# Kernel tuning notes

Hardware: AMD Instinct MI355X
Metric: run time of the kernel (lower is better)

## Reference

```python
import jax, jax.numpy as jnp
import numpy as np

K_MASK = -2.3819763e+38
B, T, D, N, K, H = 2, 4096, 2048, 8, 1, 256


def apply_rope(inputs, positions, head_dim):
    # inputs: [B, T, n, H], positions: [B, T]
    fraction = 2.0 * jnp.arange(0, head_dim // 2, dtype=jnp.float32) / head_dim
    timescale = 10000.0 ** fraction  # [H/2]
    sinusoid_inp = positions[..., None].astype(jnp.float32) / timescale  # [B,T,H/2]
    sinusoid_inp = sinusoid_inp[..., None, :]  # [B,T,1,H/2]
    sin, cos = jnp.sin(sinusoid_inp), jnp.cos(sinusoid_inp)
    first_half, second_half = jnp.split(inputs, 2, axis=-1)
    first_part = first_half * cos - second_half * sin
    second_part = second_half * cos + first_half * sin
    return jnp.concatenate([first_part, second_part], axis=-1).astype(inputs.dtype)


def setup_inputs() -> dict:
    key = jax.random.key(0)
    kx, kq, kkv, ko = jax.random.split(key, 4)
    x = jax.random.normal(kx, (B, T, D), dtype=jnp.float32)
    segment_pos = jnp.broadcast_to(jnp.arange(T, dtype=jnp.int32), (B, T))
    attn_mask = jnp.broadcast_to(
        jnp.tril(jnp.ones((T, T), dtype=bool)), (B, T, T))  # causal
    q_w = jax.random.normal(kq, (N, D, H), dtype=jnp.float32) * 0.02
    kv_w = jax.random.normal(kkv, (2, K, D, H), dtype=jnp.float32) * 0.02
    out_w = jax.random.normal(ko, (N, H, D), dtype=jnp.float32) * 0.02
    return {"x": x, "segment_pos": segment_pos, "attn_mask": attn_mask,
            "q_w": q_w, "kv_w": kv_w, "out_w": out_w}


def reference(x, segment_pos, attn_mask, q_w, kv_w, out_w):
    # Projections (GQA branch: num_kv_heads != num_heads)
    query_proj = jnp.einsum('btd,ndh->btnh', x, q_w)          # [B,T,N,H]
    kv_proj = jnp.einsum('bsd,ckdh->cbskh', x, kv_w)          # [2,B,T,K,H]
    key_proj, value_proj = kv_proj[0], kv_proj[1]

    query_proj = apply_rope(query_proj, segment_pos, head_dim=H)
    query_scaled = query_proj * H ** (-0.5)
    key_proj = apply_rope(key_proj, segment_pos, head_dim=H)

    # Repeat KV heads for GQA (num_kv_heads == 1 -> N heads)
    value_proj = jnp.repeat(value_proj, N, axis=-2)           # [B,S,N,H]
    key_proj = jnp.repeat(key_proj, N, axis=-2)               # [B,S,N,H]

    logits = jnp.einsum('btnh,bsnh->btns', query_scaled, key_proj)
    padded_logits = jnp.where(attn_mask[:, :, None, :], logits, K_MASK)
    probs = jax.nn.softmax(padded_logits, axis=-1).astype(key_proj.dtype)
    encoded = jnp.einsum('btns,bsnh->btnh', probs, value_proj)
    attn_output = jnp.einsum('btnh,nhd->btd', encoded, out_w)
    return attn_output
```

## Files before the change

### kernel.cpp

```cpp
#include <hip/hip_runtime.h>

#define T_SEQ 4096
#define D_MODEL 2048
#define N_HEADS 8
#define HDIM 256

typedef unsigned int uint32;
typedef unsigned short u16;
typedef __attribute__((ext_vector_type(8))) short short8;
typedef __attribute__((ext_vector_type(4))) float f32x4;
typedef __attribute__((ext_vector_type(4))) uint32 u32x4;

__device__ __forceinline__ float bf2f(u16 v) {
  return __uint_as_float(((uint32)v) << 16);
}
__device__ __forceinline__ u16 f2bf(float f) {
  uint32 u = __float_as_uint(f);
  u += 0x7fffu + ((u >> 16) & 1u);
  return (u16)(u >> 16);
}
__device__ __forceinline__ uint32 pkbf(float x, float y) {
  return (uint32)f2bf(x) | ((uint32)f2bf(y) << 16);
}
__device__ __forceinline__ uint2 pack4(const f32x4 v) {
  uint2 r;
  r.x = (uint32)f2bf(v[0]) | ((uint32)f2bf(v[1]) << 16);
  r.y = (uint32)f2bf(v[2]) | ((uint32)f2bf(v[3]) << 16);
  return r;
}
__device__ __forceinline__ void gload16(const u16* g, u16* l) {
  __builtin_amdgcn_global_load_lds(
      (const __attribute__((address_space(1))) unsigned int*)g,
      (__attribute__((address_space(3))) unsigned int*)l, 16, 0, 0);
}

__global__ __launch_bounds__(256) void convert_x(const float* __restrict__ x,
                                                 u16* __restrict__ xb) {
  const int idx = blockIdx.x * 256 + threadIdx.x;
  float4 v = *(const float4*)(x + (size_t)idx * 4);
  uint2 pk;
  pk.x = (uint32)f2bf(v.x) | ((uint32)f2bf(v.y) << 16);
  pk.y = (uint32)f2bf(v.z) | ((uint32)f2bf(v.w) << 16);
  *(uint2*)(xb + (size_t)idx * 4) = pk;
}

__global__ __launch_bounds__(256) void prep_weights(
    const float* __restrict__ qw, const float* __restrict__ kvw,
    const float* __restrict__ ow, u16* __restrict__ Wt, u16* __restrict__ Owt) {
  __shared__ float Ts[64][65];
  const int t = threadIdx.x;
  const int tx = blockIdx.x, ty = blockIdx.y, z = blockIdx.z;
  const float* src;
  int srcStride;
  u16* dst;
  if (z == 0) {
    const int c0 = tx * 64;
    const float* base = (c0 < 2048)
                            ? qw + (size_t)(c0 >> 8) * D_MODEL * HDIM
                            : kvw + (size_t)((c0 - 2048) >> 8) * D_MODEL * HDIM;
    src = base + (c0 & 255);
    srcStride = HDIM;
    dst = Wt + (size_t)c0 * D_MODEL;
  } else {
    if (tx >= 32) return;
    src = ow + tx * 64;
    srcStride = D_MODEL;
    dst = Owt + (size_t)tx * 64 * D_MODEL;
  }
  const int d0 = ty * 64;
  const int r = t >> 4, c4 = (t & 15) * 4;
#pragma unroll
  for (int i = 0; i < 4; ++i) {
    float4 v = *(const float4*)(src + (size_t)(d0 + r + i * 16) * srcStride + c4);
    *(float4*)&Ts[r + i * 16][c4] = v;
  }
  __syncthreads();
#pragma unroll
  for (int i = 0; i < 4; ++i) {
    const int crow = r + i * 16;
    uint2 pk;
    pk.x = (uint32)f2bf(Ts[c4 + 0][crow]) | ((uint32)f2bf(Ts[c4 + 1][crow]) << 16);
    pk.y = (uint32)f2bf(Ts[c4 + 2][crow]) | ((uint32)f2bf(Ts[c4 + 3][crow]) << 16);
    *(uint2*)(dst + (size_t)crow * D_MODEL + d0 + c4) = pk;
  }
}

__global__ __launch_bounds__(256) void gemm_qkv_mfma(
    const u16* __restrict__ xb, const u16* __restrict__ Wt,
    u16* __restrict__ Qb, u16* __restrict__ Kb, u16* __restrict__ Vt) {
  __shared__ u16 Asm[128][32];
  __shared__ u16 Bsm[128][32];
  const int t = threadIdx.x;
  const int w = t >> 6, l = t & 63, quad = l >> 4, lq = l & 15;
  const int wm = w & 1, wn = w >> 1;
  const int col0 = blockIdx.x * 128, row0 = blockIdx.y * 128;
  const u16* ga0 = xb + (size_t)(row0 + (t >> 2)) * D_MODEL + (t & 3) * 8;
  const u16* ga1 = ga0 + (size_t)64 * D_MODEL;
  const u16* gb0 = Wt + (size_t)(col0 + (t >> 2)) * D_MODEL + (t & 3) * 8;
  const u16* gb1 = gb0 + (size_t)64 * D_MODEL;
  u16* lA0 = &Asm[0][0] + t * 8;
  u16* lA1 = lA0 + 2048;
  u16* lB0 = &Bsm[0][0] + t * 8;
  u16* lB1 = lB0 + 2048;
  f32x4 acc[4][4];
#pragma unroll
  for (int i = 0; i < 4; ++i)
#pragma unroll
    for (int j = 0; j < 4; ++j) acc[i][j] = (f32x4){0.f, 0.f, 0.f, 0.f};
  for (int k0 = 0; k0 < D_MODEL; k0 += 32) {
    gload16(ga0 + k0, lA0);
    gload16(ga1 + k0, lA1);
    gload16(gb0 + k0, lB0);
    gload16(gb1 + k0, lB1);
    __syncthreads();
    short8 af[4], bf[4];
#pragma unroll
    for (int i = 0; i < 4; ++i)
      af[i] = *(const short8*)&Asm[wm * 64 + i * 16 + lq][quad * 8];
#pragma unroll
    for (int j = 0; j < 4; ++j)
      bf[j] = *(const short8*)&Bsm[wn * 64 + j * 16 + lq][quad * 8];
#pragma unroll
    for (int i = 0; i < 4; ++i)
#pragma unroll
      for (int j = 0; j < 4; ++j)
        acc[i][j] =
            __builtin_amdgcn_mfma_f32_16x16x32_bf16(af[i], bf[j], acc[i][j], 0, 0, 0);
    __syncthreads();
  }
  const int b = row0 >> 12, sbase = row0 & 4095;
#pragma unroll
  for (int i = 0; i < 4; ++i) {
    const int rowloc = wm * 64 + i * 16 + quad * 4;
#pragma unroll
    for (int j = 0; j < 4; ++j) {
      const int col = col0 + wn * 64 + j * 16 + lq;
      if (col < 2048) {
#pragma unroll
        for (int r = 0; r < 4; ++r)
          Qb[(size_t)(row0 + rowloc + r) * 2048 + col] = f2bf(acc[i][j][r]);
      } else if (col < 2304) {
#pragma unroll
        for (int r = 0; r < 4; ++r)
          Kb[(size_t)(row0 + rowloc + r) * HDIM + (col - 2048)] =
              f2bf(acc[i][j][r]);
      } else {
        *(uint2*)(Vt + ((size_t)b * HDIM + col - 2304) * T_SEQ + sbase + rowloc) =
            pack4(acc[i][j]);
      }
    }
  }
}

__global__ __launch_bounds__(256) void rope_kernel(u16* __restrict__ Qb,
                                                   u16* __restrict__ Kb,
                                                   const int* __restrict__ segpos) {
  const int bt = blockIdx.x;
  const int tid = threadIdx.x;
  const float fpos = (float)segpos[bt];
  const float k_ln = 9.210340371976184f / 128.0f;
  for (int p = tid; p < 1024; p += 256) {
    const int n = p >> 7, i = p & 127;
    const size_t base = (size_t)bt * (N_HEADS * HDIM) + (size_t)n * HDIM;
    const float th = fpos * expf(-(float)i * k_ln);
    float s, c;
    sincosf(th, &s, &c);
    const float f1 = bf2f(Qb[base + i]);
    const float f2 = bf2f(Qb[base + i + 128]);
    Qb[base + i] = f2bf((f1 * c - f2 * s) * 0.0625f);
    Qb[base + i + 128] = f2bf((f2 * c + f1 * s) * 0.0625f);
  }
  if (tid < 128) {
    const int i = tid;
    const size_t base = (size_t)bt * HDIM;
    const float th = fpos * expf(-(float)i * k_ln);
    float s, c;
    sincosf(th, &s, &c);
    const float f1 = bf2f(Kb[base + i]);
    const float f2 = bf2f(Kb[base + i + 128]);
    Kb[base + i] = f2bf(f1 * c - f2 * s);
    Kb[base + i + 128] = f2bf(f2 * c + f1 * s);
  }
}

__global__ __launch_bounds__(256, 2) void attn_mfma(const u16* __restrict__ Qb,
                                                    const u16* __restrict__ Kb,
                                                    const u16* __restrict__ Vt,
                                                    u16* __restrict__ Eb) {
  __shared__ u16 KsB[2][8192];
  __shared__ u16 VsB[2][8192];
  const int t = threadIdx.x;
  const int w = t >> 6, l = t & 63;
  const int quad = l >> 4, lq = l & 15;
  const int sx = lq & 7;
  const int bid = blockIdx.x;
  const int n = blockIdx.y, b = blockIdx.z;
  const u16* kgbase = Kb + (size_t)b * T_SEQ * HDIM;
  const u16* vgbase = Vt + (size_t)b * HDIM * T_SEQ;

  int koff[4], voff[4], ldo[4];
#pragma unroll
  for (int p = 0; p < 4; ++p) {
    const int cid = w * 4 + p;
    const int krow = 2 * cid + (l >> 5);
    const int kchk = (l & 31) ^ (krow & 7);
    koff[p] = krow * HDIM + kchk * 8;
    const int s_ = cid * 64 + l;
    const int c_ = s_ ^ ((s_ >> 3) & 7);
    voff[p] = (c_ >> 2) * T_SEQ + (c_ & 3) * 8;
    ldo[p] = cid * 512 + l * 8;
  }
  const int vlx = (lq * 32 + quad * 8) ^ ((lq >> 1) << 3);

  auto stage = [&](int buf, int s0) {
#pragma unroll
    for (int p = 0; p < 4; ++p)
      gload16(kgbase + (size_t)s0 * HDIM + koff[p], &KsB[buf][ldo[p]]);
#pragma unroll
    for (int p = 0; p < 4; ++p)
      gload16(vgbase + (size_t)voff[p] + s0, &VsB[buf][ldo[p]]);
  };

#pragma unroll 1
  for (int ti = 0; ti < 2; ++ti) {
    const int qt = ti ? bid : 63 - bid;
    const int q0 = qt * 64;
    const int wrow0 = q0 + w * 16;

    short8 qf[8];
    {
      const u16* qbase = Qb +
          (((size_t)b * T_SEQ + wrow0 + lq) * N_HEADS + n) * HDIM + quad * 8;
#pragma unroll
      for (int c = 0; c < 8; ++c) qf[c] = *(const short8*)(qbase + c * 32);
    }
    stage(0, 0);

    f32x4 O[16];
#pragma unroll
    for (int i = 0; i < 16; ++i) O[i] = (f32x4){0.f, 0.f, 0.f, 0.f};
    float m_i = -1e30f, l_i = 0.f;

    const int nst = 2 * qt + 2;
    int cur = 0;
#pragma unroll 1
    for (int st = 0; st < nst; ++st) {
      const int s0 = st * 32;
      if (st + 1 < nst) {
        stage(cur ^ 1, s0 + 32);
        asm volatile("s_waitcnt vmcnt(8)" ::: "memory");
      } else {
        asm volatile("s_waitcnt vmcnt(0)" ::: "memory");
      }
      __builtin_amdgcn_s_barrier();
      if (s0 <= wrow0 + 15) {
        const u16* Kc = &KsB[cur][0];
        f32x4 sa0 = (f32x4){0.f, 0.f, 0.f, 0.f};
        f32x4 sa1 = (f32x4){0.f, 0.f, 0.f, 0.f};
        __builtin_amdgcn_s_setprio(1);
#pragma unroll
        for (int c = 0; c < 8; ++c) {
          const int cb = ((c * 4 + quad) ^ sx) * 8;
          short8 k0 = *(const short8*)&Kc[lq * 256 + cb];
          short8 k1 = *(const short8*)&Kc[(16 + lq) * 256 + cb];
          sa0 = __builtin_amdgcn_mfma_f32_16x16x32_bf16(k0, qf[c], sa0, 0, 0, 0);
          sa1 = __builtin_amdgcn_mfma_f32_16x16x32_bf16(k1, qf[c], sa1, 0, 0, 0);
        }
        __builtin_amdgcn_s_setprio(0);
        if (s0 + 31 > wrow0) {
          const int qrow = wrow0 + lq;
#pragma unroll
          for (int r = 0; r < 4; ++r) {
            if (s0 + quad * 4 + r > qrow) sa0[r] = -1e30f;
            if (s0 + 16 + quad * 4 + r > qrow) sa1[r] = -1e30f;
          }
        }
        float mx = fmaxf(fmaxf(fmaxf(sa0[0], sa0[1]), fmaxf(sa0[2], sa0[3])),
                         fmaxf(fmaxf(sa1[0], sa1[1]), fmaxf(sa1[2], sa1[3])));
        mx = fmaxf(mx, __shfl_xor(mx, 16));
        mx = fmaxf(mx, __shfl_xor(mx, 32));
        if (!__all(mx - m_i <= 8.f)) {
          const float mnew = fmaxf(m_i, mx);
          const float a = __expf(m_i - mnew);
          l_i *= a;
          m_i = mnew;
#pragma unroll
          for (int r = 0; r < 4; ++r) {
            const float ar = __shfl(a, quad * 4 + r);
#pragma unroll
            for (int ntl = 0; ntl < 16; ++ntl) O[ntl][r] *= ar;
          }
        }
        const float p0 = __expf(sa0[0] - m_i), p1 = __expf(sa0[1] - m_i);
        const float p2 = __expf(sa0[2] - m_i), p3 = __expf(sa0[3] - m_i);
        const float p4 = __expf(sa1[0] - m_i), p5 = __expf(sa1[1] - m_i);
        const float p6 = __expf(sa1[2] - m_i), p7 = __expf(sa1[3] - m_i);
        float rs = ((p0 + p1) + (p2 + p3)) + ((p4 + p5) + (p6 + p7));
        rs += __shfl_xor(rs, 16);
        rs += __shfl_xor(rs, 32);
        l_i += rs;
        const uint32 a0 = pkbf(p0, p1), a1 = pkbf(p2, p3);
        const uint32 b0 = pkbf(p4, p5), b1 = pkbf(p6, p7);
        const uint32 s10 = (quad < 2) ? b0 : a0;
        const uint32 s11 = (quad < 2) ? b1 : a1;
        const uint32 r10 = __shfl_xor(s10, 32);
        const uint32 r11 = __shfl_xor(s11, 32);
        const bool sR = (quad == 0) || (quad == 3);
        const uint32 s20 = sR ? r10 : ((quad == 1) ? a0 : b0);
        const uint32 s21 = sR ? r11 : ((quad == 1) ? a1 : b1);
        const uint32 r20 = __shfl_xor(s20, 16);
        const uint32 r21 = __shfl_xor(s21, 16);
        const uint32 w0 = (quad == 0) ? a0 : (quad == 2) ? r10 : r20;
        const uint32 w1 = (quad == 0) ? a1 : (quad == 2) ? r11 : r21;
        const uint32 w2 = (quad == 1) ? r10 : (quad == 3) ? b0 : r20;
        const uint32 w3 = (quad == 1) ? r11 : (quad == 3) ? b1 : r21;
        const u32x4 pw = (u32x4){w0, w1, w2, w3};
        const short8 pf = __builtin_bit_cast(short8, pw);
        const u16* Vc = &VsB[cur][vlx];
        __builtin_amdgcn_s_setprio(1);
#pragma unroll
        for (int ntl = 0; ntl < 16; ++ntl) {
          short8 vf = *(const short8*)&Vc[ntl * 512];
          O[ntl] = __builtin_amdgcn_mfma_f32_16x16x32_bf16(pf, vf, O[ntl], 0, 0, 0);
        }
        __builtin_amdgcn_s_setprio(0);
      }
      __builtin_amdgcn_s_barrier();
      cur ^= 1;
    }
    const float inv = 1.0f / l_i;
    float invq[4];
#pragma unroll
    for (int r = 0; r < 4; ++r) invq[r] = __shfl(inv, quad * 4 + r);
    u16* ebase =
        Eb + (((size_t)b * T_SEQ + wrow0 + quad * 4) * N_HEADS + n) * HDIM + lq;
#pragma unroll
    for (int ntl = 0; ntl < 16; ++ntl)
#pragma unroll
      for (int r = 0; r < 4; ++r)
        ebase[(size_t)r * (N_HEADS * HDIM) + ntl * 16] = f2bf(O[ntl][r] * invq[r]);
  }
}

__global__ __launch_bounds__(256) void gemm_out_mfma(const u16* __restrict__ E,
                                                     const u16* __restrict__ Owt,
                                                     float* __restrict__ out) {
  __shared__ u16 Asm[128][32];
  __shared__ u16 Bsm[128][32];
  const int t = threadIdx.x;
  const int w = t >> 6, l = t & 63, quad = l >> 4, lq = l & 15;
  const int wm = w & 1, wn = w >> 1;
  const int col0 = blockIdx.x * 128, row0 = blockIdx.y * 128;
  const u16* ga0 = E + (size_t)(row0 + (t >> 2)) * D_MODEL + (t & 3) * 8;
  const u16* ga1 = ga0 + (size_t)64 * D_MODEL;
  const u16* gb0 = Owt + (size_t)(col0 + (t >> 2)) * D_MODEL + (t & 3) * 8;
  const u16* gb1 = gb0 + (size_t)64 * D_MODEL;
  u16* lA0 = &Asm[0][0] + t * 8;
  u16* lA1 = lA0 + 2048;
  u16* lB0 = &Bsm[0][0] + t * 8;
  u16* lB1 = lB0 + 2048;
  f32x4 acc[4][4];
#pragma unroll
  for (int i = 0; i < 4; ++i)
#pragma unroll
    for (int j = 0; j < 4; ++j) acc[i][j] = (f32x4){0.f, 0.f, 0.f, 0.f};
  for (int k0 = 0; k0 < D_MODEL; k0 += 32) {
    gload16(ga0 + k0, lA0);
    gload16(ga1 + k0, lA1);
    gload16(gb0 + k0, lB0);
    gload16(gb1 + k0, lB1);
    __syncthreads();
    short8 af[4], bf[4];
#pragma unroll
    for (int i = 0; i < 4; ++i)
      af[i] = *(const short8*)&Asm[wm * 64 + i * 16 + lq][quad * 8];
#pragma unroll
    for (int j = 0; j < 4; ++j)
      bf[j] = *(const short8*)&Bsm[wn * 64 + j * 16 + lq][quad * 8];
#pragma unroll
    for (int i = 0; i < 4; ++i)
#pragma unroll
      for (int j = 0; j < 4; ++j)
        acc[i][j] =
            __builtin_amdgcn_mfma_f32_16x16x32_bf16(af[i], bf[j], acc[i][j], 0, 0, 0);
    __syncthreads();
  }
#pragma unroll
  for (int i = 0; i < 4; ++i) {
    const int row = row0 + wm * 64 + i * 16 + quad * 4;
#pragma unroll
    for (int j = 0; j < 4; ++j) {
      const int col = col0 + wn * 64 + j * 16 + lq;
#pragma unroll
      for (int r = 0; r < 4; ++r)
        out[(size_t)(row + r) * D_MODEL + col] = acc[i][j][r];
    }
  }
}

extern "C" void kernel_launch(void* const* d_in, const int* in_sizes, int n_in,
                              void* d_out, int out_size, void* d_ws,
                              size_t ws_size, hipStream_t stream) {
  const float* x = (const float*)d_in[0];
  const int* segpos = (const int*)d_in[1];
  const float* qw = (const float*)d_in[3];
  const float* kvw = (const float*)d_in[4];
  const float* ow = (const float*)d_in[5];
  float* out = (float*)d_out;

  char* ws = (char*)d_ws;
  u16* Qb = (u16*)ws;
  u16* Kb = (u16*)(ws + (size_t)33554432);
  u16* Vt = (u16*)(ws + (size_t)37748736);
  u16* xb = (u16*)(ws + (size_t)41943040);
  u16* Eb = xb;
  u16* Wt = (u16*)(ws + (size_t)75497472);
  u16* Owt = (u16*)(ws + (size_t)85983232);

  hipLaunchKernelGGL(convert_x, dim3(16384), dim3(256), 0, stream, x, xb);
  hipLaunchKernelGGL(prep_weights, dim3(40, 32, 2), dim3(256), 0, stream, qw,
                     kvw, ow, Wt, Owt);
  hipLaunchKernelGGL(gemm_qkv_mfma, dim3(20, 64), dim3(256), 0, stream, xb, Wt,
                     Qb, Kb, Vt);
  hipLaunchKernelGGL(rope_kernel, dim3(8192), dim3(256), 0, stream, Qb, Kb,
                     segpos);
  hipLaunchKernelGGL(attn_mfma, dim3(32, N_HEADS, 2), dim3(256), 0, stream, Qb,
                     Kb, Vt, Eb);
  hipLaunchKernelGGL(gemm_out_mfma, dim3(16, 64), dim3(256), 0, stream, Eb, Owt,
                     out);
}
```

Before: 699.3 us.

## Double query rows per attention wave and swizzle GEMM block order for XCD locality

Each attention wave now processes 32 query rows (two 16-row groups) instead of 16, so every K/V tile staged into shared memory feeds twice the MFMA work. Block count halves, each block handles two 128-row tiles, and launch bounds drop to one block per SIMD to fit the doubled accumulators. The QKV and output GEMMs also remap block indices so consecutive blocks on the same XCD share tiles in cache. Risks are fewer resident waves for latency hiding, more register pressure, and fewer blocks for load balance.

```diff
diff --git a/kernel.cpp b/kernel.cpp
--- a/kernel.cpp
+++ b/kernel.cpp
@@ -93,7 +93,9 @@
   const int t = threadIdx.x;
   const int w = t >> 6, l = t & 63, quad = l >> 4, lq = l & 15;
   const int wm = w & 1, wn = w >> 1;
-  const int col0 = blockIdx.x * 128, row0 = blockIdx.y * 128;
+  const int lb = blockIdx.x + 20 * blockIdx.y;
+  const int sw = (lb & 7) * 160 + (lb >> 3);
+  const int col0 = (sw % 20) * 128, row0 = (sw / 20) * 128;
   const u16* ga0 = xb + (size_t)(row0 + (t >> 2)) * D_MODEL + (t & 3) * 8;
   const u16* ga1 = ga0 + (size_t)64 * D_MODEL;
   const u16* gb0 = Wt + (size_t)(col0 + (t >> 2)) * D_MODEL + (t & 3) * 8;
@@ -183,7 +185,7 @@
   }
 }
 
-__global__ __launch_bounds__(256, 2) void attn_mfma(const u16* __restrict__ Qb,
+__global__ __launch_bounds__(256, 1) void attn_mfma(const u16* __restrict__ Qb,
                                                     const u16* __restrict__ Kb,
                                                     const u16* __restrict__ Vt,
                                                     u16* __restrict__ Eb) {
@@ -223,25 +225,33 @@
 
 #pragma unroll 1
   for (int ti = 0; ti < 2; ++ti) {
-    const int qt = ti ? bid : 63 - bid;
-    const int q0 = qt * 64;
-    const int wrow0 = q0 + w * 16;
-
-    short8 qf[8];
+    const int qt = ti ? bid : 31 - bid;
+    const int q0 = qt * 128;
+    const int wrow0 = q0 + w * 32;
+
+    short8 qf0[8], qf1[8];
     {
-      const u16* qbase = Qb +
+      const u16* qb0 = Qb +
           (((size_t)b * T_SEQ + wrow0 + lq) * N_HEADS + n) * HDIM + quad * 8;
-#pragma unroll
-      for (int c = 0; c < 8; ++c) qf[c] = *(const short8*)(qbase + c * 32);
+      const u16* qb1 = qb0 + (size_t)16 * N_HEADS * HDIM;
+#pragma unroll
+      for (int c = 0; c < 8; ++c) {
+        qf0[c] = *(const short8*)(qb0 + c * 32);
+        qf1[c] = *(const short8*)(qb1 + c * 32);
+      }
     }
     stage(0, 0);
 
-    f32x4 O[16];
-#pragma unroll
-    for (int i = 0; i < 16; ++i) O[i] = (f32x4){0.f, 0.f, 0.f, 0.f};
-    float m_i = -1e30f, l_i = 0.f;
-
-    const int nst = 2 * qt + 2;
+    f32x4 O0[16], O1[16];
+#pragma unroll
+    for (int i = 0; i < 16; ++i) {
+      O0[i] = (f32x4){0.f, 0.f, 0.f, 0.f};
+      O1[i] = (f32x4){0.f, 0.f, 0.f, 0.f};
+    }
+    float m0 = -1e30f, li0 = 0.f;
+    float m1 = -1e30f, li1 = 0.f;
+
+    const int nst = 4 * qt + 4;
     int cur = 0;
 #pragma unroll 1
     for (int st = 0; st < nst; ++st) {
@@ -253,92 +263,170 @@
         asm volatile("s_waitcnt vmcnt(0)" ::: "memory");
       }
       __builtin_amdgcn_s_barrier();
-      if (s0 <= wrow0 + 15) {
+      if (s0 <= wrow0 + 31) {
         const u16* Kc = &KsB[cur][0];
-        f32x4 sa0 = (f32x4){0.f, 0.f, 0.f, 0.f};
-        f32x4 sa1 = (f32x4){0.f, 0.f, 0.f, 0.f};
+        f32x4 sa00 = (f32x4){0.f, 0.f, 0.f, 0.f};
+        f32x4 sa01 = (f32x4){0.f, 0.f, 0.f, 0.f};
+        f32x4 sa10 = (f32x4){0.f, 0.f, 0.f, 0.f};
+        f32x4 sa11 = (f32x4){0.f, 0.f, 0.f, 0.f};
         __builtin_amdgcn_s_setprio(1);
 #pragma unroll
         for (int c = 0; c < 8; ++c) {
           const int cb = ((c * 4 + quad) ^ sx) * 8;
           short8 k0 = *(const short8*)&Kc[lq * 256 + cb];
           short8 k1 = *(const short8*)&Kc[(16 + lq) * 256 + cb];
-          sa0 = __builtin_amdgcn_mfma_f32_16x16x32_bf16(k0, qf[c], sa0, 0, 0, 0);
-          sa1 = __builtin_amdgcn_mfma_f32_16x16x32_bf16(k1, qf[c], sa1, 0, 0, 0);
+          sa00 = __builtin_amdgcn_mfma_f32_16x16x32_bf16(k0, qf0[c], sa00, 0, 0, 0);
+          sa01 = __builtin_amdgcn_mfma_f32_16x16x32_bf16(k1, qf0[c], sa01, 0, 0, 0);
+          sa10 = __builtin_amdgcn_mfma_f32_16x16x32_bf16(k0, qf1[c], sa10, 0, 0, 0);
+          sa11 = __builtin_amdgcn_mfma_f32_16x16x32_bf16(k1, qf1[c], sa11, 0, 0, 0);
         }
         __builtin_amdgcn_s_setprio(0);
         if (s0 + 31 > wrow0) {
           const int qrow = wrow0 + lq;
 #pragma unroll
           for (int r = 0; r < 4; ++r) {
-            if (s0 + quad * 4 + r > qrow) sa0[r] = -1e30f;
-            if (s0 + 16 + quad * 4 + r > qrow) sa1[r] = -1e30f;
+            if (s0 + quad * 4 + r > qrow) sa00[r] = -1e30f;
+            if (s0 + 16 + quad * 4 + r > qrow) sa01[r] = -1e30f;
           }
         }
-        float mx = fmaxf(fmaxf(fmaxf(sa0[0], sa0[1]), fmaxf(sa0[2], sa0[3])),
-                         fmaxf(fmaxf(sa1[0], sa1[1]), fmaxf(sa1[2], sa1[3])));
-        mx = fmaxf(mx, __shfl_xor(mx, 16));
-        mx = fmaxf(mx, __shfl_xor(mx, 32));
-        if (!__all(mx - m_i <= 8.f)) {
-          const float mnew = fmaxf(m_i, mx);
-          const float a = __expf(m_i - mnew);
-          l_i *= a;
-          m_i = mnew;
+        if (s0 + 15 > wrow0) {
+          const int qrow = wrow0 + 16 + lq;
+#pragma unroll
+          for (int r = 0; r < 4; ++r) {
+            if (s0 + quad * 4 + r > qrow) sa10[r] = -1e30f;
+            if (s0 + 16 + quad * 4 + r > qrow) sa11[r] = -1e30f;
+          }
+        }
+        float mx0 = fmaxf(fmaxf(fmaxf(sa00[0], sa00[1]), fmaxf(sa00[2], sa00[3])),
+                          fmaxf(fmaxf(sa01[0], sa01[1]), fmaxf(sa01[2], sa01[3])));
+        mx0 = fmaxf(mx0, __shfl_xor(mx0, 16));
+        mx0 = fmaxf(mx0, __shfl_xor(mx0, 32));
+        if (!__all(mx0 - m0 <= 8.f)) {
+          const float mnew = fmaxf(m0, mx0);
+          const float a = __expf(m0 - mnew);
+          li0 *= a;
+          m0 = mnew;
 #pragma unroll
           for (int r = 0; r < 4; ++r) {
             const float ar = __shfl(a, quad * 4 + r);
 #pragma unroll
-            for (int ntl = 0; ntl < 16; ++ntl) O[ntl][r] *= ar;
+            for (int ntl = 0; ntl < 16; ++ntl) O0[ntl][r] *= ar;
           }
         }
-        const float p0 = __expf(sa0[0] - m_i), p1 = __expf(sa0[1] - m_i);
-        const float p2 = __expf(sa0[2] - m_i), p3 = __expf(sa0[3] - m_i);
-        const float p4 = __expf(sa1[0] - m_i), p5 = __expf(sa1[1] - m_i);
-        const float p6 = __expf(sa1[2] - m_i), p7 = __expf(sa1[3] - m_i);
-        float rs = ((p0 + p1) + (p2 + p3)) + ((p4 + p5) + (p6 + p7));
-        rs += __shfl_xor(rs, 16);
-        rs += __shfl_xor(rs, 32);
-        l_i += rs;
-        const uint32 a0 = pkbf(p0, p1), a1 = pkbf(p2, p3);
-        const uint32 b0 = pkbf(p4, p5), b1 = pkbf(p6, p7);
-        const uint32 s10 = (quad < 2) ? b0 : a0;
-        const uint32 s11 = (quad < 2) ? b1 : a1;
-        const uint32 r10 = __shfl_xor(s10, 32);
-        const uint32 r11 = __shfl_xor(s11, 32);
-        const bool sR = (quad == 0) || (quad == 3);
-        const uint32 s20 = sR ? r10 : ((quad == 1) ? a0 : b0);
-        const uint32 s21 = sR ? r11 : ((quad == 1) ? a1 : b1);
-        const uint32 r20 = __shfl_xor(s20, 16);
-        const uint32 r21 = __shfl_xor(s21, 16);
-        const uint32 w0 = (quad == 0) ? a0 : (quad == 2) ? r10 : r20;
-        const uint32 w1 = (quad == 0) ? a1 : (quad == 2) ? r11 : r21;
-        const uint32 w2 = (quad == 1) ? r10 : (quad == 3) ? b0 : r20;
-        const uint32 w3 = (quad == 1) ? r11 : (quad == 3) ? b1 : r21;
-        const u32x4 pw = (u32x4){w0, w1, w2, w3};
-        const short8 pf = __builtin_bit_cast(short8, pw);
+        const float g0p0 = __expf(sa00[0] - m0), g0p1 = __expf(sa00[1] - m0);
+        const float g0p2 = __expf(sa00[2] - m0), g0p3 = __expf(sa00[3] - m0);
+        const float g0p4 = __expf(sa01[0] - m0), g0p5 = __expf(sa01[1] - m0);
+        const float g0p6 = __expf(sa01[2] - m0), g0p7 = __expf(sa01[3] - m0);
+        {
+          float rs = ((g0p0 + g0p1) + (g0p2 + g0p3)) + ((g0p4 + g0p5) + (g0p6 + g0p7));
+          rs += __shfl_xor(rs, 16);
+          rs += __shfl_xor(rs, 32);
+          li0 += rs;
+        }
+        float mx1 = fmaxf(fmaxf(fmaxf(sa10[0], sa10[1]), fmaxf(sa10[2], sa10[3])),
+                          fmaxf(fmaxf(sa11[0], sa11[1]), fmaxf(sa11[2], sa11[3])));
+        mx1 = fmaxf(mx1, __shfl_xor(mx1, 16));
+        mx1 = fmaxf(mx1, __shfl_xor(mx1, 32));
+        if (!__all(mx1 - m1 <= 8.f)) {
+          const float mnew = fmaxf(m1, mx1);
+          const float a = __expf(m1 - mnew);
+          li1 *= a;
+          m1 = mnew;
+#pragma unroll
+          for (int r = 0; r < 4; ++r) {
+            const float ar = __shfl(a, quad * 4 + r);
+#pragma unroll
+            for (int ntl = 0; ntl < 16; ++ntl) O1[ntl][r] *= ar;
+          }
+        }
+        const float g1p0 = __expf(sa10[0] - m1), g1p1 = __expf(sa10[1] - m1);
+        const float g1p2 = __expf(sa10[2] - m1), g1p3 = __expf(sa10[3] - m1);
+        const float g1p4 = __expf(sa11[0] - m1), g1p5 = __expf(sa11[1] - m1);
+        const float g1p6 = __expf(sa11[2] - m1), g1p7 = __expf(sa11[3] - m1);
+        {
+          float rs = ((g1p0 + g1p1) + (g1p2 + g1p3)) + ((g1p4 + g1p5) + (g1p6 + g1p7));
+          rs += __shfl_xor(rs, 16);
+          rs += __shfl_xor(rs, 32);
+          li1 += rs;
+        }
+        short8 pf0, pf1;
+        {
+          const uint32 a0 = pkbf(g0p0, g0p1), a1 = pkbf(g0p2, g0p3);
+          const uint32 b0 = pkbf(g0p4, g0p5), b1 = pkbf(g0p6, g0p7);
+          const uint32 s10 = (quad < 2) ? b0 : a0;
+          const uint32 s11 = (quad < 2) ? b1 : a1;
+          const uint32 r10 = __shfl_xor(s10, 32);
+          const uint32 r11 = __shfl_xor(s11, 32);
+          const bool sR = (quad == 0) || (quad == 3);
+          const uint32 s20 = sR ? r10 : ((quad == 1) ? a0 : b0);
+          const uint32 s21 = sR ? r11 : ((quad == 1) ? a1 : b1);
+          const uint32 r20 = __shfl_xor(s20, 16);
+          const uint32 r21 = __shfl_xor(s21, 16);
+          const uint32 w0 = (quad == 0) ? a0 : (quad == 2) ? r10 : r20;
+          const uint32 w1 = (quad == 0) ? a1 : (quad == 2) ? r11 : r21;
+          const uint32 w2 = (quad == 1) ? r10 : (quad == 3) ? b0 : r20;
+          const uint32 w3 = (quad == 1) ? r11 : (quad == 3) ? b1 : r21;
+          const u32x4 pw = (u32x4){w0, w1, w2, w3};
+          pf0 = __builtin_bit_cast(short8, pw);
+        }
+        {
+          const uint32 a0 = pkbf(g1p0, g1p1), a1 = pkbf(g1p2, g1p3);
+          const uint32 b0 = pkbf(g1p4, g1p5), b1 = pkbf(g1p6, g1p7);
+          const uint32 s10 = (quad < 2) ? b0 : a0;
+          const uint32 s11 = (quad < 2) ? b1 : a1;
+          const uint32 r10 = __shfl_xor(s10, 32);
+          const uint32 r11 = __shfl_xor(s11, 32);
+          const bool sR = (quad == 0) || (quad == 3);
+          const uint32 s20 = sR ? r10 : ((quad == 1) ? a0 : b0);
+          const uint32 s21 = sR ? r11 : ((quad == 1) ? a1 : b1);
+          const uint32 r20 = __shfl_xor(s20, 16);
+          const uint32 r21 = __shfl_xor(s21, 16);
+          const uint32 w0 = (quad == 0) ? a0 : (quad == 2) ? r10 : r20;
+          const uint32 w1 = (quad == 0) ? a1 : (quad == 2) ? r11 : r21;
+          const uint32 w2 = (quad == 1) ? r10 : (quad == 3) ? b0 : r20;
+          const uint32 w3 = (quad == 1) ? r11 : (quad == 3) ? b1 : r21;
+          const u32x4 pw = (u32x4){w0, w1, w2, w3};
+          pf1 = __builtin_bit_cast(short8, pw);
+        }
         const u16* Vc = &VsB[cur][vlx];
         __builtin_amdgcn_s_setprio(1);
 #pragma unroll
         for (int ntl = 0; ntl < 16; ++ntl) {
           short8 vf = *(const short8*)&Vc[ntl * 512];
-          O[ntl] = __builtin_amdgcn_mfma_f32_16x16x32_bf16(pf, vf, O[ntl], 0, 0, 0);
+          O0[ntl] = __builtin_amdgcn_mfma_f32_16x16x32_bf16(pf0, vf, O0[ntl], 0, 0, 0);
+          O1[ntl] = __builtin_amdgcn_mfma_f32_16x16x32_bf16(pf1, vf, O1[ntl], 0, 0, 0);
         }
         __builtin_amdgcn_s_setprio(0);
       }
       __builtin_amdgcn_s_barrier();
       cur ^= 1;
     }
-    const float inv = 1.0f / l_i;
-    float invq[4];
-#pragma unroll
-    for (int r = 0; r < 4; ++r) invq[r] = __shfl(inv, quad * 4 + r);
-    u16* ebase =
-        Eb + (((size_t)b * T_SEQ + wrow0 + quad * 4) * N_HEADS + n) * HDIM + lq;
-#pragma unroll
-    for (int ntl = 0; ntl < 16; ++ntl)
-#pragma unroll
-      for (int r = 0; r < 4; ++r)
-        ebase[(size_t)r * (N_HEADS * HDIM) + ntl * 16] = f2bf(O[ntl][r] * invq[r]);
+    {
+      const float inv = 1.0f / li0;
+      float invq[4];
+#pragma unroll
+      for (int r = 0; r < 4; ++r) invq[r] = __shfl(inv, quad * 4 + r);
+      u16* ebase =
+          Eb + (((size_t)b * T_SEQ + wrow0 + quad * 4) * N_HEADS + n) * HDIM + lq;
+#pragma unroll
+      for (int ntl = 0; ntl < 16; ++ntl)
+#pragma unroll
+        for (int r = 0; r < 4; ++r)
+          ebase[(size_t)r * (N_HEADS * HDIM) + ntl * 16] = f2bf(O0[ntl][r] * invq[r]);
+    }
+    {
+      const float inv = 1.0f / li1;
+      float invq[4];
+#pragma unroll
+      for (int r = 0; r < 4; ++r) invq[r] = __shfl(inv, quad * 4 + r);
+      u16* ebase =
+          Eb + (((size_t)b * T_SEQ + wrow0 + 16 + quad * 4) * N_HEADS + n) * HDIM + lq;
+#pragma unroll
+      for (int ntl = 0; ntl < 16; ++ntl)
+#pragma unroll
+        for (int r = 0; r < 4; ++r)
+          ebase[(size_t)r * (N_HEADS * HDIM) + ntl * 16] = f2bf(O1[ntl][r] * invq[r]);
+    }
   }
 }
 
@@ -350,7 +438,9 @@
   const int t = threadIdx.x;
   const int w = t >> 6, l = t & 63, quad = l >> 4, lq = l & 15;
   const int wm = w & 1, wn = w >> 1;
-  const int col0 = blockIdx.x * 128, row0 = blockIdx.y * 128;
+  const int lb = blockIdx.x + 16 * blockIdx.y;
+  const int sw = (lb & 7) * 128 + (lb >> 3);
+  const int col0 = (sw % 16) * 128, row0 = (sw / 16) * 128;
   const u16* ga0 = E + (size_t)(row0 + (t >> 2)) * D_MODEL + (t & 3) * 8;
   const u16* ga1 = ga0 + (size_t)64 * D_MODEL;
   const u16* gb0 = Owt + (size_t)(col0 + (t >> 2)) * D_MODEL + (t & 3) * 8;
@@ -424,7 +514,7 @@
                      Qb, Kb, Vt);
   hipLaunchKernelGGL(rope_kernel, dim3(8192), dim3(256), 0, stream, Qb, Kb,
                      segpos);
-  hipLaunchKernelGGL(attn_mfma, dim3(32, N_HEADS, 2), dim3(256), 0, stream, Qb,
+  hipLaunchKernelGGL(attn_mfma, dim3(16, N_HEADS, 2), dim3(256), 0, stream, Qb,
                      Kb, Vt, Eb);
   hipLaunchKernelGGL(gemm_out_mfma, dim3(16, 64), dim3(256), 0, stream, Eb, Owt,
                      out);
```

Result: slower. 783.8 us (+12.1%).

## Rewrite projection GEMMs with 256x256 tiles, double-buffered LDS and XOR swizzle

Applied to the files above, without the earlier changes.

Both the QKV projection and output projection GEMMs now share a core that uses 256x256 block tiles with 512 threads, a double-buffered LDS ring whose global loads for the next K-step overlap the MFMA work on the current one, and an XOR swizzle on the LDS chunk index to avoid bank conflicts. Block indices are remapped so that consecutive blocks spread across tiles, which is meant to improve L2 reuse, and s_setprio is raised around the MFMA bursts. The aim is to cut global-load latency stalls and redundant operand traffic in the GEMM phases. In exchange, register pressure goes up (32 accumulators per thread) and the launch grid gets coarser.

```diff
diff --git a/kernel.cpp b/kernel.cpp
--- a/kernel.cpp
+++ b/kernel.cpp
@@ -85,71 +85,154 @@
   }
 }
 
-__global__ __launch_bounds__(256) void gemm_qkv_mfma(
+__device__ __forceinline__ void gemm256_core(const u16* __restrict__ A,
+                                             const u16* __restrict__ B,
+                                             int row0, int col0,
+                                             u16 (&SB)[2][16384],
+                                             f32x4 (&acc)[8][4]) {
+  const int t = threadIdx.x;
+  const int l = t & 63, quad = l >> 4, lq = l & 15;
+  const int w = t >> 6, wm = w >> 2, wn = w & 3;
+  const int crow = t >> 2;
+  const int cch = ((t & 3) ^ ((t >> 3) & 3)) * 8;
+  const u16* pA0 = A + (size_t)(row0 + crow) * 2048 + cch;
+  const u16* pA1 = pA0 + (size_t)128 * 2048;
+  const u16* pB0 = B + (size_t)(col0 + crow) * 2048 + cch;
+  const u16* pB1 = pB0 + (size_t)128 * 2048;
+  const int t8 = t * 8;
+  const int ckk = (quad ^ ((lq >> 1) & 3)) * 8;
+  const int aBase = (wm * 128 + lq) * 32 + ckk;
+  const int bBase = 8192 + (wn * 64 + lq) * 32 + ckk;
+
+  gload16(pA0, &SB[0][t8]);
+  gload16(pA1, &SB[0][4096 + t8]);
+  gload16(pB0, &SB[0][8192 + t8]);
+  gload16(pB1, &SB[0][12288 + t8]);
+#pragma unroll
+  for (int i = 0; i < 8; ++i)
+#pragma unroll
+    for (int j = 0; j < 4; ++j) acc[i][j] = (f32x4){0.f, 0.f, 0.f, 0.f};
+
+  int cur = 0;
+#pragma unroll 1
+  for (int kt = 0; kt < 64; ++kt) {
+    const int kn = (kt + 1) * 32;
+    short8 bf[4];
+    if (kt < 63) {
+      gload16(pA0 + kn, &SB[cur ^ 1][t8]);
+      gload16(pA1 + kn, &SB[cur ^ 1][4096 + t8]);
+      asm volatile("s_waitcnt vmcnt(2)" ::: "memory");
+    } else {
+      asm volatile("s_waitcnt vmcnt(0)" ::: "memory");
+    }
+    __builtin_amdgcn_s_barrier();
+    {
+      const u16* S = &SB[cur][0];
+      short8 af[4];
+#pragma unroll
+      for (int i = 0; i < 4; ++i) af[i] = *(const short8*)&S[aBase + i * 512];
+#pragma unroll
+      for (int j = 0; j < 4; ++j) bf[j] = *(const short8*)&S[bBase + j * 512];
+      __builtin_amdgcn_s_setprio(1);
+#pragma unroll
+      for (int i = 0; i < 4; ++i)
+#pragma unroll
+        for (int j = 0; j < 4; ++j)
+          acc[i][j] =
+              __builtin_amdgcn_mfma_f32_16x16x32_bf16(af[i], bf[j], acc[i][j], 0, 0, 0);
+      __builtin_amdgcn_s_setprio(0);
+    }
+    if (kt < 63) {
+      gload16(pB0 + kn, &SB[cur ^ 1][8192 + t8]);
+      gload16(pB1 + kn, &SB[cur ^ 1][12288 + t8]);
+    }
+    {
+      const u16* S = &SB[cur][0];
+      short8 af[4];
+#pragma unroll
+      for (int i = 0; i < 4; ++i)
+        af[i] = *(const short8*)&S[aBase + (4 + i) * 512];
+      __builtin_amdgcn_s_setprio(1);
+#pragma unroll
+      for (int i = 0; i < 4; ++i)
+#pragma unroll
+        for (int j = 0; j < 4; ++j)
+          acc[4 + i][j] =
+              __builtin_amdgcn_mfma_f32_16x16x32_bf16(af[i], bf[j], acc[4 + i][j], 0, 0, 0);
+      __builtin_amdgcn_s_setprio(0);
+    }
+    __builtin_amdgcn_s_barrier();
+    cur ^= 1;
+  }
+}
+
+__global__ __launch_bounds__(512, 2) void gemm_qkv_mfma(
     const u16* __restrict__ xb, const u16* __restrict__ Wt,
     u16* __restrict__ Qb, u16* __restrict__ Kb, u16* __restrict__ Vt) {
-  __shared__ u16 Asm[128][32];
-  __shared__ u16 Bsm[128][32];
+  __shared__ u16 SB[2][16384];
+  const int lb = blockIdx.x + 10 * blockIdx.y;
+  const int sw = (lb & 7) * 40 + (lb >> 3);
+  const int col0 = (sw % 10) * 256, row0 = (sw / 10) * 256;
+  f32x4 acc[8][4];
+  gemm256_core(xb, Wt, row0, col0, SB, acc);
+
   const int t = threadIdx.x;
-  const int w = t >> 6, l = t & 63, quad = l >> 4, lq = l & 15;
-  const int wm = w & 1, wn = w >> 1;
-  const int col0 = blockIdx.x * 128, row0 = blockIdx.y * 128;
-  const u16* ga0 = xb + (size_t)(row0 + (t >> 2)) * D_MODEL + (t & 3) * 8;
-  const u16* ga1 = ga0 + (size_t)64 * D_MODEL;
-  const u16* gb0 = Wt + (size_t)(col0 + (t >> 2)) * D_MODEL + (t & 3) * 8;
-  const u16* gb1 = gb0 + (size_t)64 * D_MODEL;
-  u16* lA0 = &Asm[0][0] + t * 8;
-  u16* lA1 = lA0 + 2048;
-  u16* lB0 = &Bsm[0][0] + t * 8;
-  u16* lB1 = lB0 + 2048;
-  f32x4 acc[4][4];
-#pragma unroll
-  for (int i = 0; i < 4; ++i)
-#pragma unroll
-    for (int j = 0; j < 4; ++j) acc[i][j] = (f32x4){0.f, 0.f, 0.f, 0.f};
-  for (int k0 = 0; k0 < D_MODEL; k0 += 32) {
-    gload16(ga0 + k0, lA0);
-    gload16(ga1 + k0, lA1);
-    gload16(gb0 + k0, lB0);
-    gload16(gb1 + k0, lB1);
-    __syncthreads();
-    short8 af[4], bf[4];
-#pragma unroll
-    for (int i = 0; i < 4; ++i)
-      af[i] = *(const short8*)&Asm[wm * 64 + i * 16 + lq][quad * 8];
-#pragma unroll
-    for (int j = 0; j < 4; ++j)
-      bf[j] = *(const short8*)&Bsm[wn * 64 + j * 16 + lq][quad * 8];
-#pragma unroll
-    for (int i = 0; i < 4; ++i)
-#pragma unroll
-      for (int j = 0; j < 4; ++j)
-        acc[i][j] =
-            __builtin_amdgcn_mfma_f32_16x16x32_bf16(af[i], bf[j], acc[i][j], 0, 0, 0);
-    __syncthreads();
-  }
-  const int b = row0 >> 12, sbase = row0 & 4095;
-#pragma unroll
-  for (int i = 0; i < 4; ++i) {
-    const int rowloc = wm * 64 + i * 16 + quad * 4;
-#pragma unroll
-    for (int j = 0; j < 4; ++j) {
-      const int col = col0 + wn * 64 + j * 16 + lq;
-      if (col < 2048) {
+  const int l = t & 63, quad = l >> 4, lq = l & 15;
+  const int w = t >> 6, wm = w >> 2, wn = w & 3;
+  const int rl = wm * 128 + quad * 4;
+  const int cl = wn * 64 + lq;
+  if (col0 < 2048) {
+#pragma unroll
+    for (int mf = 0; mf < 8; ++mf)
+#pragma unroll
+      for (int nf = 0; nf < 4; ++nf)
 #pragma unroll
         for (int r = 0; r < 4; ++r)
-          Qb[(size_t)(row0 + rowloc + r) * 2048 + col] = f2bf(acc[i][j][r]);
-      } else if (col < 2304) {
+          Qb[(size_t)(row0 + rl + mf * 16 + r) * 2048 + col0 + cl + nf * 16] =
+              f2bf(acc[mf][nf][r]);
+  } else if (col0 == 2048) {
+#pragma unroll
+    for (int mf = 0; mf < 8; ++mf)
+#pragma unroll
+      for (int nf = 0; nf < 4; ++nf)
 #pragma unroll
         for (int r = 0; r < 4; ++r)
-          Kb[(size_t)(row0 + rowloc + r) * HDIM + (col - 2048)] =
-              f2bf(acc[i][j][r]);
-      } else {
-        *(uint2*)(Vt + ((size_t)b * HDIM + col - 2304) * T_SEQ + sbase + rowloc) =
-            pack4(acc[i][j]);
-      }
-    }
-  }
+          Kb[(size_t)(row0 + rl + mf * 16 + r) * HDIM + cl + nf * 16] =
+              f2bf(acc[mf][nf][r]);
+  } else {
+    const int b = row0 >> 12, sb = row0 & 4095;
+#pragma unroll
+    for (int mf = 0; mf < 8; ++mf)
+#pragma unroll
+      for (int nf = 0; nf < 4; ++nf)
+        *(uint2*)(Vt + ((size_t)b * HDIM + cl + nf * 16) * T_SEQ + sb + rl +
+                  mf * 16) = pack4(acc[mf][nf]);
+  }
+}
+
+__global__ __launch_bounds__(512, 2) void gemm_out_mfma(
+    const u16* __restrict__ E, const u16* __restrict__ Owt,
+    float* __restrict__ out) {
+  __shared__ u16 SB[2][16384];
+  const int lb = blockIdx.x + 8 * blockIdx.y;
+  const int sw = (lb & 7) * 32 + (lb >> 3);
+  const int col0 = (sw % 8) * 256, row0 = (sw / 8) * 256;
+  f32x4 acc[8][4];
+  gemm256_core(E, Owt, row0, col0, SB, acc);
+
+  const int t = threadIdx.x;
+  const int l = t & 63, quad = l >> 4, lq = l & 15;
+  const int w = t >> 6, wm = w >> 2, wn = w & 3;
+  const int rl = wm * 128 + quad * 4;
+  const int cl = wn * 64 + lq;
+#pragma unroll
+  for (int mf = 0; mf < 8; ++mf)
+#pragma unroll
+    for (int nf = 0; nf < 4; ++nf)
+#pragma unroll
+      for (int r = 0; r < 4; ++r)
+        out[(size_t)(row0 + rl + mf * 16 + r) * 2048 + col0 + cl + nf * 16] =
+            acc[mf][nf][r];
 }
 
 __global__ __launch_bounds__(256) void rope_kernel(u16* __restrict__ Qb,
@@ -342,62 +425,6 @@
   }
 }
 
-__global__ __launch_bounds__(256) void gemm_out_mfma(const u16* __restrict__ E,
-                                                     const u16* __restrict__ Owt,
-                                                     float* __restrict__ out) {
-  __shared__ u16 Asm[128][32];
-  __shared__ u16 Bsm[128][32];
-  const int t = threadIdx.x;
-  const int w = t >> 6, l = t & 63, quad = l >> 4, lq = l & 15;
-  const int wm = w & 1, wn = w >> 1;
-  const int col0 = blockIdx.x * 128, row0 = blockIdx.y * 128;
-  const u16* ga0 = E + (size_t)(row0 + (t >> 2)) * D_MODEL + (t & 3) * 8;
-  const u16* ga1 = ga0 + (size_t)64 * D_MODEL;
-  const u16* gb0 = Owt + (size_t)(col0 + (t >> 2)) * D_MODEL + (t & 3) * 8;
-  const u16* gb1 = gb0 + (size_t)64 * D_MODEL;
-  u16* lA0 = &Asm[0][0] + t * 8;
-  u16* lA1 = lA0 + 2048;
-  u16* lB0 = &Bsm[0][0] + t * 8;
-  u16* lB1 = lB0 + 2048;
-  f32x4 acc[4][4];
-#pragma unroll
-  for (int i = 0; i < 4; ++i)
-#pragma unroll
-    for (int j = 0; j < 4; ++j) acc[i][j] = (f32x4){0.f, 0.f, 0.f, 0.f};
-  for (int k0 = 0; k0 < D_MODEL; k0 += 32) {
-    gload16(ga0 + k0, lA0);
-    gload16(ga1 + k0, lA1);
-    gload16(gb0 + k0, lB0);
-    gload16(gb1 + k0, lB1);
-    __syncthreads();
-    short8 af[4], bf[4];
-#pragma unroll
-    for (int i = 0; i < 4; ++i)
-      af[i] = *(const short8*)&Asm[wm * 64 + i * 16 + lq][quad * 8];
-#pragma unroll
-    for (int j = 0; j < 4; ++j)
-      bf[j] = *(const short8*)&Bsm[wn * 64 + j * 16 + lq][quad * 8];
-#pragma unroll
-    for (int i = 0; i < 4; ++i)
-#pragma unroll
-      for (int j = 0; j < 4; ++j)
-        acc[i][j] =
-            __builtin_amdgcn_mfma_f32_16x16x32_bf16(af[i], bf[j], acc[i][j], 0, 0, 0);
-    __syncthreads();
-  }
-#pragma unroll
-  for (int i = 0; i < 4; ++i) {
-    const int row = row0 + wm * 64 + i * 16 + quad * 4;
-#pragma unroll
-    for (int j = 0; j < 4; ++j) {
-      const int col = col0 + wn * 64 + j * 16 + lq;
-#pragma unroll
-      for (int r = 0; r < 4; ++r)
-        out[(size_t)(row + r) * D_MODEL + col] = acc[i][j][r];
-    }
-  }
-}
-
 extern "C" void kernel_launch(void* const* d_in, const int* in_sizes, int n_in,
                               void* d_out, int out_size, void* d_ws,
                               size_t ws_size, hipStream_t stream) {
@@ -420,12 +447,12 @@
   hipLaunchKernelGGL(convert_x, dim3(16384), dim3(256), 0, stream, x, xb);
   hipLaunchKernelGGL(prep_weights, dim3(40, 32, 2), dim3(256), 0, stream, qw,
                      kvw, ow, Wt, Owt);
-  hipLaunchKernelGGL(gemm_qkv_mfma, dim3(20, 64), dim3(256), 0, stream, xb, Wt,
+  hipLaunchKernelGGL(gemm_qkv_mfma, dim3(10, 32), dim3(512), 0, stream, xb, Wt,
                      Qb, Kb, Vt);
   hipLaunchKernelGGL(rope_kernel, dim3(8192), dim3(256), 0, stream, Qb, Kb,
                      segpos);
   hipLaunchKernelGGL(attn_mfma, dim3(32, N_HEADS, 2), dim3(256), 0, stream, Qb,
                      Kb, Vt, Eb);
-  hipLaunchKernelGGL(gemm_out_mfma, dim3(16, 64), dim3(256), 0, stream, Eb, Owt,
+  hipLaunchKernelGGL(gemm_out_mfma, dim3(8, 32), dim3(512), 0, stream, Eb, Owt,
                      out);
 }
```

Result: faster. 663.6 us (-5.1%).
